# Kernel optimization log

Hardware: AMD Instinct MI355X
Metric: run time of the kernel (lower is better)

## Reference

```python
import math
import jax, jax.numpy as jnp
import numpy as np

B, S, D = 2, 2048, 1024
H, DK = 16, 64
NUM_BUCKETS = 32
MAX_DISTANCE = 128


def _relative_position_bucket(relative_position, num_buckets=NUM_BUCKETS, max_distance=MAX_DISTANCE):
    # bidirectional=True branch (encoder / non-causal)
    n = -relative_position
    num_buckets = num_buckets // 2
    ret = (n < 0).astype(jnp.int32) * num_buckets
    n = jnp.abs(n)
    max_exact = num_buckets // 2
    is_small = n < max_exact
    # guard log(0); masked out by is_small anyway
    n_safe = jnp.maximum(n, 1).astype(jnp.float32)
    val_if_large = max_exact + (
        jnp.log(n_safe / max_exact) / math.log(max_distance / max_exact) * (num_buckets - max_exact)
    ).astype(jnp.int32)
    val_if_large = jnp.minimum(val_if_large, num_buckets - 1)
    return ret + jnp.where(is_small, n, val_if_large)


def setup_inputs() -> dict:
    key = jax.random.key(0)
    ks = jax.random.split(key, 6)
    std_q = (D * DK) ** -0.5
    std = D ** -0.5
    return {
        "x": jax.random.normal(ks[0], (B, S, D), jnp.float32),
        "q_w": jax.random.normal(ks[1], (H * DK, D), jnp.float32) * std_q,
        "k_w": jax.random.normal(ks[2], (H * DK, D), jnp.float32) * std,
        "v_w": jax.random.normal(ks[3], (H * DK, D), jnp.float32) * std,
        "o_w": jax.random.normal(ks[4], (D, H * DK), jnp.float32) * ((H * DK) ** -0.5),
        "rel_bias": jax.random.normal(ks[5], (NUM_BUCKETS, H), jnp.float32) * std,
    }


def reference(x, q_w, k_w, v_w, o_w, rel_bias):
    b, s, _ = x.shape
    # project and split heads: [B, H, S, DK]
    def proj(w):
        return (x @ w.T).reshape(b, s, H, DK).transpose(0, 2, 1, 3)
    q, k, v = proj(q_w), proj(k_w), proj(v_w)

    # T5-style unscaled attention scores: [B, H, Sq, Sk]
    scores = jnp.einsum("bhqd,bhkd->bhqk", q, k)

    # bucketed relative-position bias
    ctx = jnp.arange(s)[:, None]
    mem = jnp.arange(s)[None, :]
    rp_bucket = _relative_position_bucket(mem - ctx)  # [S, S]
    bias = rel_bias[rp_bucket]                        # [S, S, H]
    bias = bias.transpose(2, 0, 1)[None]              # [1, H, S, S]
    scores = scores + bias

    attn = jax.nn.softmax(scores, axis=-1)
    ctx_out = jnp.einsum("bhqk,bhkd->bhqd", attn, v)
    ctx_out = ctx_out.transpose(0, 2, 1, 3).reshape(b, s, H * DK)
    return ctx_out @ o_w.T
```

## Files before the change

kernel.cpp:

```cpp
#include <hip/hip_runtime.h>
#include <stdint.h>


typedef unsigned short u16;
typedef __attribute__((ext_vector_type(8))) short short8;
typedef __attribute__((ext_vector_type(4))) float float4v;
typedef __attribute__((ext_vector_type(4))) u16 ushort4v;

typedef __attribute__((address_space(1))) void void_g;
typedef __attribute__((address_space(3))) void void_l;

#define L2E 1.4426950408889634f

__device__ __forceinline__ u16 f2b(float f) {
  union { float f; uint32_t u; } v; v.f = f;
  uint32_t r = (v.u + 0x7fffu + ((v.u >> 16) & 1u)) >> 16;
  return (u16)r;
}
__device__ __forceinline__ u16 f2b_fast(float f) {
  union { float f; uint32_t u; } v; v.f = f;
  return (u16)((v.u + 0x8000u) >> 16);
}

__global__ void cvt_all(const float* __restrict__ x,  const float* __restrict__ qw,
                        const float* __restrict__ kw, const float* __restrict__ vw,
                        const float* __restrict__ ow, const float* __restrict__ rel_bias,
                        u16* __restrict__ xb, u16* __restrict__ wqkv, u16* __restrict__ owb,
                        float* __restrict__ biasT) {
  int bi = blockIdx.x;
  if (bi >= 8192) {
    int idx = (bi - 8192) * 256 + threadIdx.x;
    int h = idx >> 12, t = idx & 4095;
    if (t > 4094) { biasT[h * 4096 + 4095] = -1.0e4f; return; }
    int d = t - 2047;
    int n = -d;
    int ret = (n < 0) ? 16 : 0;
    int na = (n < 0) ? -n : n;
    int bucket;
    if (na < 8) {
      bucket = ret + na;
    } else {
      float v = logf((float)na / 8.0f) / logf(16.0f) * 8.0f;
      int vi = 8 + (int)v;
      bucket = ret + (vi > 15 ? 15 : vi);
    }
    biasT[h * 4096 + t] = (rel_bias[bucket * 16 + h] - 8.0f) * L2E;
    return;
  }
  int i = bi * 256 + threadIdx.x;
  const float* s; u16* d; int off;
  if (i < 1048576)      { s = x;  d = xb;              off = i; }
  else if (i < 1310720) { s = qw; d = wqkv;            off = i - 1048576; }
  else if (i < 1572864) { s = kw; d = wqkv + 1048576;  off = i - 1310720; }
  else if (i < 1835008) { s = vw; d = wqkv + 2097152;  off = i - 1572864; }
  else                  { s = ow; d = owb;             off = i - 1835008; }
  float4v v = ((const float4v*)s)[off];
  ushort4v o;
  o.x = f2b(v.x); o.y = f2b(v.y); o.z = f2b(v.z); o.w = f2b(v.w);
  ((ushort4v*)d)[off] = o;
}

template<bool OUT_BF16>
__global__ __launch_bounds__(256, 2)
void gemm_bt(const u16* __restrict__ A, const u16* __restrict__ W,
             void* __restrict__ Cp, int K, int N) {
  __shared__ __align__(16) char SM[34816];
  u16* As = (u16*)SM;
  u16* Bs = (u16*)(SM + 16384);
  const int tid = threadIdx.x;
  const int wid = tid >> 6;
  const int lane = tid & 63;
  const int row16 = lane & 15, oct = lane >> 4;
  const int tm = blockIdx.x * 128, tn = blockIdx.y * 128;
  const int wm = (wid & 1) * 64, wn = (wid >> 1) * 64;
  const int srow = lane >> 2;
  const int sc = (lane & 3) * 8;
  float4v acc[4][4] = {};
  for (int k0 = 0; k0 < K; k0 += 64) {
    __syncthreads();
#pragma unroll
    for (int i = 0; i < 4; i++) {
      const int idx = i * 4 + wid;
      const int kk = idx & 1;
      const int rb = idx >> 1;
      const int r = rb * 16 + srow;
      const int c = kk * 32 + sc;
      __builtin_amdgcn_global_load_lds((void_g*)(A + (size_t)(tm + r) * K + k0 + c),
                                       (void_l*)(As + (kk * 128 + rb * 16) * 32), 16, 0, 0);
      __builtin_amdgcn_global_load_lds((void_g*)(W + (size_t)(tn + r) * K + k0 + c),
                                       (void_l*)(Bs + (kk * 128 + rb * 16) * 32), 16, 0, 0);
    }
    __syncthreads();
#pragma unroll
    for (int kk = 0; kk < 2; kk++) {
      short8 af[4], bfr[4];
#pragma unroll
      for (int mi = 0; mi < 4; mi++)
        af[mi] = *(const short8*)(As + (kk * 128 + wm + mi * 16 + row16) * 32 + oct * 8);
#pragma unroll
      for (int ni = 0; ni < 4; ni++)
        bfr[ni] = *(const short8*)(Bs + (kk * 128 + wn + ni * 16 + row16) * 32 + oct * 8);
#pragma unroll
      for (int mi = 0; mi < 4; mi++)
#pragma unroll
        for (int ni = 0; ni < 4; ni++)
          acc[mi][ni] = __builtin_amdgcn_mfma_f32_16x16x32_bf16(af[mi], bfr[ni], acc[mi][ni], 0, 0, 0);
    }
  }

  if (OUT_BF16) {
    u16* Es = (u16*)SM;
    __syncthreads();
#pragma unroll
    for (int mi = 0; mi < 4; mi++)
#pragma unroll
      for (int ni = 0; ni < 4; ni++)
#pragma unroll
        for (int r = 0; r < 4; r++)
          Es[(wm + mi * 16 + oct * 4 + r) * 136 + wn + ni * 16 + row16] = f2b(acc[mi][ni][r]);
    __syncthreads();
    u16* C = (u16*)Cp;
#pragma unroll
    for (int it = 0; it < 8; it++) {
      int idx = it * 256 + tid;
      int row = idx >> 4, c = idx & 15;
      short8 v = *(const short8*)(Es + row * 136 + c * 8);
      *(short8*)(C + (size_t)(tm + row) * N + tn + c * 8) = v;
    }
  } else {
    float* Ef = (float*)SM;
    float* C = (float*)Cp;
#pragma unroll
    for (int pass = 0; pass < 2; pass++) {
      __syncthreads();
      if ((wid & 1) == pass) {
#pragma unroll
        for (int mi = 0; mi < 4; mi++)
#pragma unroll
          for (int ni = 0; ni < 4; ni++)
#pragma unroll
            for (int r = 0; r < 4; r++)
              Ef[(mi * 16 + oct * 4 + r) * 132 + wn + ni * 16 + row16] = acc[mi][ni][r];
      }
      __syncthreads();
#pragma unroll
      for (int it = 0; it < 8; it++) {
        int idx = it * 256 + tid;
        int row = idx >> 5, c = idx & 31;
        float4v v = *(const float4v*)(Ef + row * 132 + c * 4);
        *(float4v*)(C + (size_t)(tm + pass * 64 + row) * N + tn + c * 4) = v;
      }
    }
  }
}

__global__ __launch_bounds__(256, 2)
void transpose_v(const u16* __restrict__ QKV, u16* __restrict__ vTp) {
  const int s0 = blockIdx.x * 64, h = blockIdx.y, b = blockIdx.z;
  const int tid = threadIdx.x;
  __shared__ u16 T[64 * 73];
  const u16* src = QKV + 2048 + (size_t)b * 2048 * 3072 + h * 64;
#pragma unroll
  for (int it = 0; it < 2; it++) {
    int idx = it * 256 + tid;
    int sl = idx >> 3;
    int c = idx & 7;
    short8 v = *(const short8*)(src + (size_t)(s0 + sl) * 3072 + c * 8);
#pragma unroll
    for (int k = 0; k < 8; k++) T[(c * 8 + k) * 73 + sl] = (u16)v[k];
  }
  __syncthreads();
  u16* dst = vTp + ((size_t)(b * 16 + h) * 64) * 2048 + s0;
#pragma unroll
  for (int it = 0; it < 2; it++) {
    int idx = it * 256 + tid;
    int d = idx >> 3;
    int cs = idx & 7;
    short8 o;
#pragma unroll
    for (int k = 0; k < 8; k++) {
      int sp = cs * 8 + k;
      int sl = (sp & 32) + 16 * (sp & 1) + ((sp & 31) >> 1);
      o[k] = (short)T[d * 73 + sl];
    }
    *(short8*)(dst + (size_t)d * 2048 + cs * 8) = o;
  }
}

__global__ __launch_bounds__(256, 2)
void flash_attn(const u16* __restrict__ QKV, const u16* __restrict__ vTp,
                const float* __restrict__ biasT, u16* __restrict__ ctx) {
  const int S = 2048, LDQ = 3072;
  const int qt0 = blockIdx.x * 128;
  const int h = blockIdx.y, b = blockIdx.z;
  const int tid = threadIdx.x, wid = tid >> 6, lane = tid & 63;
  const int row16 = lane & 15, oct = lane >> 4;

  __shared__ __align__(16) float biasS[2176];
  __shared__ __align__(16) u16 Ks[2][64][40];
  __shared__ __align__(16) u16 Vts[2][64][40];
  __shared__ __align__(16) u16 Pl[4][2][16][40];

  {
    const float* bsrc = biasT + h * 4096 + (1920 - qt0);
    for (int i = tid; i < 544; i += 256)
      ((float4v*)biasS)[i] = ((const float4v*)bsrc)[i];
  }

  const u16* qbase = QKV + ((size_t)b * S + qt0 + wid * 32) * LDQ + h * 64;
  short8 qf[2][2];
#pragma unroll
  for (int f = 0; f < 2; f++)
#pragma unroll
    for (int hd = 0; hd < 2; hd++)
      qf[f][hd] = *(const short8*)(qbase + (size_t)(f * 16 + row16) * LDQ + hd * 32 + oct * 8);

  float l_r[2][4] = {};
  float4v o_acc[2][4] = {};

  const int sr = lane >> 2, c8 = (lane & 3) * 8;
  const int srow = wid * 16 + sr;
  const u16* Kst = QKV + 1024 + ((size_t)b * S + srow) * LDQ + h * 64 + c8;
  const u16* Vst = vTp + ((size_t)(b * 16 + h) * 64 + srow) * 2048 + c8;

  short8 kreg[2], vreg[2];
#pragma unroll
  for (int hd = 0; hd < 2; hd++) kreg[hd] = *(const short8*)(Kst + hd * 32);
#pragma unroll
  for (int ks = 0; ks < 2; ks++) vreg[ks] = *(const short8*)(Vst + ks * 32);

  for (int kt = 0; kt < S; kt += 64) {
    __syncthreads();
#pragma unroll
    for (int hd = 0; hd < 2; hd++) *(short8*)&Ks[hd][srow][c8] = kreg[hd];
#pragma unroll
    for (int ks = 0; ks < 2; ks++) *(short8*)&Vts[ks][srow][c8] = vreg[ks];
    __syncthreads();

    if (kt + 64 < S) {
#pragma unroll
      for (int hd = 0; hd < 2; hd++)
        kreg[hd] = *(const short8*)(Kst + (size_t)(kt + 64) * LDQ + hd * 32);
#pragma unroll
      for (int ks = 0; ks < 2; ks++)
        vreg[ks] = *(const short8*)(Vst + (kt + 64) + ks * 32);
    }

    short8 kf[4][2];
#pragma unroll
    for (int st = 0; st < 4; st++)
#pragma unroll
      for (int hd = 0; hd < 2; hd++)
        kf[st][hd] = *(const short8*)&Ks[hd][st * 16 + row16][oct * 8];

    float4v sc[2][4];
#pragma unroll
    for (int f = 0; f < 2; f++)
#pragma unroll
      for (int st = 0; st < 4; st++) {
        float4v s = {};
        s = __builtin_amdgcn_mfma_f32_16x16x32_bf16(qf[f][0], kf[st][0], s, 0, 0, 0);
        s = __builtin_amdgcn_mfma_f32_16x16x32_bf16(qf[f][1], kf[st][1], s, 0, 0, 0);
        sc[f][st] = s;
      }

    short8 vf[2][4];
#pragma unroll
    for (int ks = 0; ks < 2; ks++)
#pragma unroll
      for (int ni = 0; ni < 4; ni++)
        vf[ks][ni] = *(const short8*)&Vts[ks][ni * 16 + row16][oct * 8];

#pragma unroll
    for (int f = 0; f < 2; f++) {
      const int base = kt + row16 - wid * 32 - f * 16 - oct * 4 + 127;
#pragma unroll
      for (int r = 0; r < 4; r++) {
        const int i0 = base - r;
        float b0 = biasS[i0],      b1 = biasS[i0 + 16];
        float b2 = biasS[i0 + 32], b3 = biasS[i0 + 48];
        sc[f][0][r] = __builtin_amdgcn_exp2f(__builtin_fmaf(sc[f][0][r], L2E, b0));
        sc[f][1][r] = __builtin_amdgcn_exp2f(__builtin_fmaf(sc[f][1][r], L2E, b1));
        sc[f][2][r] = __builtin_amdgcn_exp2f(__builtin_fmaf(sc[f][2][r], L2E, b2));
        sc[f][3][r] = __builtin_amdgcn_exp2f(__builtin_fmaf(sc[f][3][r], L2E, b3));
      }
      if (f == 0) {
#pragma unroll
        for (int ks = 0; ks < 2; ks++)
#pragma unroll
          for (int r = 0; r < 4; r++) {
            uint32_t pk = (uint32_t)f2b_fast(sc[0][2 * ks][r]) |
                          ((uint32_t)f2b_fast(sc[0][2 * ks + 1][r]) << 16);
            *(uint32_t*)&Pl[wid][ks][oct * 4 + r][2 * row16] = pk;
          }
      }
    }
#pragma unroll
    for (int f = 0; f < 2; f++) {
      if (f == 1) {
#pragma unroll
        for (int ks = 0; ks < 2; ks++)
#pragma unroll
          for (int r = 0; r < 4; r++) {
            uint32_t pk = (uint32_t)f2b_fast(sc[1][2 * ks][r]) |
                          ((uint32_t)f2b_fast(sc[1][2 * ks + 1][r]) << 16);
            *(uint32_t*)&Pl[wid][ks][oct * 4 + r][2 * row16] = pk;
          }
      }
#pragma unroll
      for (int r = 0; r < 4; r++)
        l_r[f][r] += (sc[f][0][r] + sc[f][1][r]) + (sc[f][2][r] + sc[f][3][r]);
#pragma unroll
      for (int ks = 0; ks < 2; ks++) {
        short8 pf = *(const short8*)&Pl[wid][ks][row16][oct * 8];
#pragma unroll
        for (int ni = 0; ni < 4; ni++)
          o_acc[f][ni] = __builtin_amdgcn_mfma_f32_16x16x32_bf16(pf, vf[ks][ni], o_acc[f][ni], 0, 0, 0);
      }
    }
  }

#pragma unroll
  for (int f = 0; f < 2; f++) {
#pragma unroll
    for (int r = 0; r < 4; r++) {
      float v = l_r[f][r];
      v += __shfl_xor(v, 1); v += __shfl_xor(v, 2);
      v += __shfl_xor(v, 4); v += __shfl_xor(v, 8);
      l_r[f][r] = 1.0f / v;
    }
    const size_t orow = (size_t)b * S + qt0 + wid * 32 + f * 16 + oct * 4;
#pragma unroll
    for (int ni = 0; ni < 4; ni++)
#pragma unroll
      for (int r = 0; r < 4; r++)
        ctx[(orow + r) * 1024 + h * 64 + ni * 16 + row16] = f2b_fast(o_acc[f][ni][r] * l_r[f][r]);
  }
}

extern "C" void kernel_launch(void* const* d_in, const int* in_sizes, int n_in,
                              void* d_out, int out_size, void* d_ws, size_t ws_size,
                              hipStream_t stream) {
  const float* x        = (const float*)d_in[0];
  const float* q_w      = (const float*)d_in[1];
  const float* k_w      = (const float*)d_in[2];
  const float* v_w      = (const float*)d_in[3];
  const float* o_w      = (const float*)d_in[4];
  const float* rel_bias = (const float*)d_in[5];

  char* ws = (char*)d_ws;
  u16*   xb    = (u16*)(ws);
  u16*   wqkv  = (u16*)(ws + 8388608);
  u16*   owb   = (u16*)(ws + 14680064);
  u16*   qkvb  = (u16*)(ws + 16777216);
  u16*   ctxb  = (u16*)(ws + 41943040);
  float* biasT = (float*)(ws + 50331648);
  u16*   vTp   = xb;

  cvt_all<<<8448, 256, 0, stream>>>(x, q_w, k_w, v_w, o_w, rel_bias,
                                    xb, wqkv, owb, biasT);

  dim3 g1(4096 / 128, 3072 / 128);
  gemm_bt<true><<<g1, 256, 0, stream>>>(xb, wqkv, qkvb, 1024, 3072);

  dim3 gt(2048 / 64, 16, 2);
  transpose_v<<<gt, 256, 0, stream>>>(qkvb, vTp);

  dim3 g2(2048 / 128, 16, 2);
  flash_attn<<<g2, 256, 0, stream>>>(qkvb, vTp, biasT, ctxb);

  dim3 g3(4096 / 128, 1024 / 128);
  gemm_bt<false><<<g3, 256, 0, stream>>>(ctxb, owb, d_out, 1024, 1024);
}
```

Before: 195.8 us.

## Fuse V transpose into QKV GEMM epilogue and use constant bias for far tiles

The QKV GEMM now writes Q/K to a compact buffer and writes V directly in the transposed, permuted layout from its LDS epilogue, which removes the separate transpose_v kernel launch and its read/write pass over V. The attention kernel also detects key tiles far from the query tile, where every relative-position bucket saturates, and applies a single scalar bias there instead of indexed LDS bias loads. This adds a per-tile branch, and the GEMM epilogue does strided LDS reads for the V tiles.

```diff
diff --git a/kernel.cpp b/kernel.cpp
--- a/kernel.cpp
+++ b/kernel.cpp
@@ -60,10 +60,10 @@
   ((ushort4v*)d)[off] = o;
 }
 
-template<bool OUT_BF16>
 __global__ __launch_bounds__(256, 2)
-void gemm_bt(const u16* __restrict__ A, const u16* __restrict__ W,
-             void* __restrict__ Cp, int K, int N) {
+void gemm_qkv(const u16* __restrict__ A, const u16* __restrict__ W,
+              u16* __restrict__ qkb, u16* __restrict__ vTp) {
+  const int K = 1024;
   __shared__ __align__(16) char SM[34816];
   u16* As = (u16*)SM;
   u16* Bs = (u16*)(SM + 16384);
@@ -108,89 +108,122 @@
     }
   }
 
-  if (OUT_BF16) {
-    u16* Es = (u16*)SM;
-    __syncthreads();
-#pragma unroll
-    for (int mi = 0; mi < 4; mi++)
-#pragma unroll
-      for (int ni = 0; ni < 4; ni++)
-#pragma unroll
-        for (int r = 0; r < 4; r++)
-          Es[(wm + mi * 16 + oct * 4 + r) * 136 + wn + ni * 16 + row16] = f2b(acc[mi][ni][r]);
-    __syncthreads();
-    u16* C = (u16*)Cp;
+  u16* Es = (u16*)SM;
+  __syncthreads();
+#pragma unroll
+  for (int mi = 0; mi < 4; mi++)
+#pragma unroll
+    for (int ni = 0; ni < 4; ni++)
+#pragma unroll
+      for (int r = 0; r < 4; r++)
+        Es[(wm + mi * 16 + oct * 4 + r) * 136 + wn + ni * 16 + row16] = f2b(acc[mi][ni][r]);
+  __syncthreads();
+
+  if (tn < 2048) {
 #pragma unroll
     for (int it = 0; it < 8; it++) {
       int idx = it * 256 + tid;
       int row = idx >> 4, c = idx & 15;
       short8 v = *(const short8*)(Es + row * 136 + c * 8);
-      *(short8*)(C + (size_t)(tm + row) * N + tn + c * 8) = v;
+      *(short8*)(qkb + (size_t)(tm + row) * 2048 + tn + c * 8) = v;
     }
   } else {
-    float* Ef = (float*)SM;
-    float* C = (float*)Cp;
-#pragma unroll
-    for (int pass = 0; pass < 2; pass++) {
-      __syncthreads();
-      if ((wid & 1) == pass) {
-#pragma unroll
-        for (int mi = 0; mi < 4; mi++)
-#pragma unroll
-          for (int ni = 0; ni < 4; ni++)
-#pragma unroll
-            for (int r = 0; r < 4; r++)
-              Ef[(mi * 16 + oct * 4 + r) * 132 + wn + ni * 16 + row16] = acc[mi][ni][r];
-      }
-      __syncthreads();
-#pragma unroll
-      for (int it = 0; it < 8; it++) {
-        int idx = it * 256 + tid;
-        int row = idx >> 5, c = idx & 31;
-        float4v v = *(const float4v*)(Ef + row * 132 + c * 4);
-        *(float4v*)(C + (size_t)(tm + pass * 64 + row) * N + tn + c * 4) = v;
-      }
+    const int h0 = (tn - 2048) >> 6;
+    const int b = tm >> 11;
+    const int s0 = tm & 2047;
+#pragma unroll
+    for (int it = 0; it < 8; it++) {
+      int idx = it * 256 + tid;
+      int dg = idx >> 4;
+      int ch = idx & 15;
+      short8 o;
+#pragma unroll
+      for (int j = 0; j < 8; j++) {
+        int sp = ch * 8 + j;
+        int sl = (sp & ~31) + 16 * (sp & 1) + ((sp & 31) >> 1);
+        o[j] = (short)Es[sl * 136 + dg];
+      }
+      const int head = h0 + (dg >> 6), d = dg & 63;
+      *(short8*)(vTp + ((size_t)((b * 16 + head) * 64 + d)) * 2048 + s0 + ch * 8) = o;
     }
   }
 }
 
 __global__ __launch_bounds__(256, 2)
-void transpose_v(const u16* __restrict__ QKV, u16* __restrict__ vTp) {
-  const int s0 = blockIdx.x * 64, h = blockIdx.y, b = blockIdx.z;
+void gemm_out(const u16* __restrict__ A, const u16* __restrict__ W,
+              float* __restrict__ C) {
+  const int K = 1024, N = 1024;
+  __shared__ __align__(16) char SM[34816];
+  u16* As = (u16*)SM;
+  u16* Bs = (u16*)(SM + 16384);
   const int tid = threadIdx.x;
-  __shared__ u16 T[64 * 73];
-  const u16* src = QKV + 2048 + (size_t)b * 2048 * 3072 + h * 64;
-#pragma unroll
-  for (int it = 0; it < 2; it++) {
-    int idx = it * 256 + tid;
-    int sl = idx >> 3;
-    int c = idx & 7;
-    short8 v = *(const short8*)(src + (size_t)(s0 + sl) * 3072 + c * 8);
-#pragma unroll
-    for (int k = 0; k < 8; k++) T[(c * 8 + k) * 73 + sl] = (u16)v[k];
-  }
-  __syncthreads();
-  u16* dst = vTp + ((size_t)(b * 16 + h) * 64) * 2048 + s0;
-#pragma unroll
-  for (int it = 0; it < 2; it++) {
-    int idx = it * 256 + tid;
-    int d = idx >> 3;
-    int cs = idx & 7;
-    short8 o;
-#pragma unroll
-    for (int k = 0; k < 8; k++) {
-      int sp = cs * 8 + k;
-      int sl = (sp & 32) + 16 * (sp & 1) + ((sp & 31) >> 1);
-      o[k] = (short)T[d * 73 + sl];
-    }
-    *(short8*)(dst + (size_t)d * 2048 + cs * 8) = o;
+  const int wid = tid >> 6;
+  const int lane = tid & 63;
+  const int row16 = lane & 15, oct = lane >> 4;
+  const int tm = blockIdx.x * 128, tn = blockIdx.y * 128;
+  const int wm = (wid & 1) * 64, wn = (wid >> 1) * 64;
+  const int srow = lane >> 2;
+  const int sc = (lane & 3) * 8;
+  float4v acc[4][4] = {};
+  for (int k0 = 0; k0 < K; k0 += 64) {
+    __syncthreads();
+#pragma unroll
+    for (int i = 0; i < 4; i++) {
+      const int idx = i * 4 + wid;
+      const int kk = idx & 1;
+      const int rb = idx >> 1;
+      const int r = rb * 16 + srow;
+      const int c = kk * 32 + sc;
+      __builtin_amdgcn_global_load_lds((void_g*)(A + (size_t)(tm + r) * K + k0 + c),
+                                       (void_l*)(As + (kk * 128 + rb * 16) * 32), 16, 0, 0);
+      __builtin_amdgcn_global_load_lds((void_g*)(W + (size_t)(tn + r) * K + k0 + c),
+                                       (void_l*)(Bs + (kk * 128 + rb * 16) * 32), 16, 0, 0);
+    }
+    __syncthreads();
+#pragma unroll
+    for (int kk = 0; kk < 2; kk++) {
+      short8 af[4], bfr[4];
+#pragma unroll
+      for (int mi = 0; mi < 4; mi++)
+        af[mi] = *(const short8*)(As + (kk * 128 + wm + mi * 16 + row16) * 32 + oct * 8);
+#pragma unroll
+      for (int ni = 0; ni < 4; ni++)
+        bfr[ni] = *(const short8*)(Bs + (kk * 128 + wn + ni * 16 + row16) * 32 + oct * 8);
+#pragma unroll
+      for (int mi = 0; mi < 4; mi++)
+#pragma unroll
+        for (int ni = 0; ni < 4; ni++)
+          acc[mi][ni] = __builtin_amdgcn_mfma_f32_16x16x32_bf16(af[mi], bfr[ni], acc[mi][ni], 0, 0, 0);
+    }
+  }
+  float* Ef = (float*)SM;
+#pragma unroll
+  for (int pass = 0; pass < 2; pass++) {
+    __syncthreads();
+    if ((wid & 1) == pass) {
+#pragma unroll
+      for (int mi = 0; mi < 4; mi++)
+#pragma unroll
+        for (int ni = 0; ni < 4; ni++)
+#pragma unroll
+          for (int r = 0; r < 4; r++)
+            Ef[(mi * 16 + oct * 4 + r) * 132 + wn + ni * 16 + row16] = acc[mi][ni][r];
+    }
+    __syncthreads();
+#pragma unroll
+    for (int it = 0; it < 8; it++) {
+      int idx = it * 256 + tid;
+      int row = idx >> 5, c = idx & 31;
+      float4v v = *(const float4v*)(Ef + row * 132 + c * 4);
+      *(float4v*)(C + (size_t)(tm + pass * 64 + row) * N + tn + c * 4) = v;
+    }
   }
 }
 
 __global__ __launch_bounds__(256, 2)
-void flash_attn(const u16* __restrict__ QKV, const u16* __restrict__ vTp,
+void flash_attn(const u16* __restrict__ qkb, const u16* __restrict__ vTp,
                 const float* __restrict__ biasT, u16* __restrict__ ctx) {
-  const int S = 2048, LDQ = 3072;
+  const int S = 2048, LDQ = 2048;
   const int qt0 = blockIdx.x * 128;
   const int h = blockIdx.y, b = blockIdx.z;
   const int tid = threadIdx.x, wid = tid >> 6, lane = tid & 63;
@@ -206,8 +239,10 @@
     for (int i = tid; i < 544; i += 256)
       ((float4v*)biasS)[i] = ((const float4v*)bsrc)[i];
   }
-
-  const u16* qbase = QKV + ((size_t)b * S + qt0 + wid * 32) * LDQ + h * 64;
+  const float bias_neg = biasT[h * 4096];
+  const float bias_pos = biasT[h * 4096 + 4094];
+
+  const u16* qbase = qkb + ((size_t)b * S + qt0 + wid * 32) * LDQ + h * 64;
   short8 qf[2][2];
 #pragma unroll
   for (int f = 0; f < 2; f++)
@@ -220,7 +255,7 @@
 
   const int sr = lane >> 2, c8 = (lane & 3) * 8;
   const int srow = wid * 16 + sr;
-  const u16* Kst = QKV + 1024 + ((size_t)b * S + srow) * LDQ + h * 64 + c8;
+  const u16* Kst = qkb + 1024 + ((size_t)b * S + srow) * LDQ + c8 + h * 64;
   const u16* Vst = vTp + ((size_t)(b * 16 + h) * 64 + srow) * 2048 + c8;
 
   short8 kreg[2], vreg[2];
@@ -271,30 +306,42 @@
       for (int ni = 0; ni < 4; ni++)
         vf[ks][ni] = *(const short8*)&Vts[ks][ni * 16 + row16][oct * 8];
 
-#pragma unroll
-    for (int f = 0; f < 2; f++) {
-      const int base = kt + row16 - wid * 32 - f * 16 - oct * 4 + 127;
+    const int dk = kt - qt0;
+    const bool far = (dk >= 256) || (dk <= -192);
+    if (far) {
+      const float bc = (dk > 0) ? bias_pos : bias_neg;
+#pragma unroll
+      for (int f = 0; f < 2; f++)
+#pragma unroll
+        for (int st = 0; st < 4; st++)
+#pragma unroll
+          for (int r = 0; r < 4; r++)
+            sc[f][st][r] = __builtin_amdgcn_exp2f(__builtin_fmaf(sc[f][st][r], L2E, bc));
+    } else {
+#pragma unroll
+      for (int f = 0; f < 2; f++) {
+        const int base = kt + row16 - wid * 32 - f * 16 - oct * 4 + 127;
+#pragma unroll
+        for (int r = 0; r < 4; r++) {
+          const int i0 = base - r;
+          float b0 = biasS[i0],      b1 = biasS[i0 + 16];
+          float b2 = biasS[i0 + 32], b3 = biasS[i0 + 48];
+          sc[f][0][r] = __builtin_amdgcn_exp2f(__builtin_fmaf(sc[f][0][r], L2E, b0));
+          sc[f][1][r] = __builtin_amdgcn_exp2f(__builtin_fmaf(sc[f][1][r], L2E, b1));
+          sc[f][2][r] = __builtin_amdgcn_exp2f(__builtin_fmaf(sc[f][2][r], L2E, b2));
+          sc[f][3][r] = __builtin_amdgcn_exp2f(__builtin_fmaf(sc[f][3][r], L2E, b3));
+        }
+      }
+    }
+
+#pragma unroll
+    for (int ks = 0; ks < 2; ks++)
 #pragma unroll
       for (int r = 0; r < 4; r++) {
-        const int i0 = base - r;
-        float b0 = biasS[i0],      b1 = biasS[i0 + 16];
-        float b2 = biasS[i0 + 32], b3 = biasS[i0 + 48];
-        sc[f][0][r] = __builtin_amdgcn_exp2f(__builtin_fmaf(sc[f][0][r], L2E, b0));
-        sc[f][1][r] = __builtin_amdgcn_exp2f(__builtin_fmaf(sc[f][1][r], L2E, b1));
-        sc[f][2][r] = __builtin_amdgcn_exp2f(__builtin_fmaf(sc[f][2][r], L2E, b2));
-        sc[f][3][r] = __builtin_amdgcn_exp2f(__builtin_fmaf(sc[f][3][r], L2E, b3));
-      }
-      if (f == 0) {
-#pragma unroll
-        for (int ks = 0; ks < 2; ks++)
-#pragma unroll
-          for (int r = 0; r < 4; r++) {
-            uint32_t pk = (uint32_t)f2b_fast(sc[0][2 * ks][r]) |
-                          ((uint32_t)f2b_fast(sc[0][2 * ks + 1][r]) << 16);
-            *(uint32_t*)&Pl[wid][ks][oct * 4 + r][2 * row16] = pk;
-          }
-      }
-    }
+        uint32_t pk = (uint32_t)f2b_fast(sc[0][2 * ks][r]) |
+                      ((uint32_t)f2b_fast(sc[0][2 * ks + 1][r]) << 16);
+        *(uint32_t*)&Pl[wid][ks][oct * 4 + r][2 * row16] = pk;
+      }
 #pragma unroll
     for (int f = 0; f < 2; f++) {
       if (f == 1) {
@@ -352,23 +399,20 @@
   u16*   xb    = (u16*)(ws);
   u16*   wqkv  = (u16*)(ws + 8388608);
   u16*   owb   = (u16*)(ws + 14680064);
-  u16*   qkvb  = (u16*)(ws + 16777216);
+  u16*   qkb   = (u16*)(ws + 16777216);
+  u16*   vTp   = (u16*)(ws + 33554432);
   u16*   ctxb  = (u16*)(ws + 41943040);
   float* biasT = (float*)(ws + 50331648);
-  u16*   vTp   = xb;
 
   cvt_all<<<8448, 256, 0, stream>>>(x, q_w, k_w, v_w, o_w, rel_bias,
                                     xb, wqkv, owb, biasT);
 
   dim3 g1(4096 / 128, 3072 / 128);
-  gemm_bt<true><<<g1, 256, 0, stream>>>(xb, wqkv, qkvb, 1024, 3072);
-
-  dim3 gt(2048 / 64, 16, 2);
-  transpose_v<<<gt, 256, 0, stream>>>(qkvb, vTp);
+  gemm_qkv<<<g1, 256, 0, stream>>>(xb, wqkv, qkb, vTp);
 
   dim3 g2(2048 / 128, 16, 2);
-  flash_attn<<<g2, 256, 0, stream>>>(qkvb, vTp, biasT, ctxb);
+  flash_attn<<<g2, 256, 0, stream>>>(qkb, vTp, biasT, ctxb);
 
   dim3 g3(4096 / 128, 1024 / 128);
-  gemm_bt<false><<<g3, 256, 0, stream>>>(ctxb, owb, d_out, 1024, 1024);
-}
+  gemm_out<<<g3, 256, 0, stream>>>(ctxb, owb, (float*)d_out);
+}
```

Measured after the change: 195.5 us. No clear change (-0.1%).
